# Kernel tuning notes

Hardware: AMD Instinct MI355X
Metric: run time of the kernel (lower is better)

The kernel has to match this reference:

```python
import jax, jax.numpy as jnp
import numpy as np

INPUT_SIZE = 256
HIDDEN_SIZE = 512
OUTPUT_SIZE = 256
SEQ_LEN = 32768


def setup_inputs() -> dict:
    key = jax.random.key(0)
    k_x, k_wx, k_wh, k_wy = jax.random.split(key, 4)
    x = jax.random.normal(k_x, (SEQ_LEN, INPUT_SIZE), dtype=jnp.float32)
    Wx = jax.random.normal(k_wx, (HIDDEN_SIZE, INPUT_SIZE), dtype=jnp.float32) * np.sqrt(2.0 / (INPUT_SIZE + HIDDEN_SIZE))
    Wh = jax.random.normal(k_wh, (HIDDEN_SIZE, HIDDEN_SIZE), dtype=jnp.float32) * np.sqrt(1.0 / HIDDEN_SIZE)
    Wy = jax.random.normal(k_wy, (OUTPUT_SIZE, HIDDEN_SIZE), dtype=jnp.float32) * np.sqrt(2.0 / (HIDDEN_SIZE + OUTPUT_SIZE))
    bh = jnp.zeros((HIDDEN_SIZE, 1), dtype=jnp.float32)
    by = jnp.zeros((OUTPUT_SIZE, 1), dtype=jnp.float32)
    return {"x": x, "Wx": Wx, "Wh": Wh, "Wy": Wy, "bh": bh, "by": by}


def reference(x, Wx, Wh, Wy, bh, by):
    # x: [T, I]; Wx: [H, I]; Wh: [H, H]; Wy: [O, H]; bh: [H,1]; by: [O,1]
    bh_v = bh[:, 0]  # [H]
    by_v = by[:, 0]  # [O]
    h0 = jnp.zeros((Wh.shape[0],), dtype=x.dtype)

    def step(h, x_t):
        # h_t = tanh(Wx @ x_t + Wh @ h_{t-1} + bh)
        h_new = jnp.tanh(Wx @ x_t + Wh @ h + bh_v)
        return h_new, h_new

    _, h_hist = jax.lax.scan(step, h0, x)  # [T, H]
    # y_t = Wy @ h_t + by, concatenated and flattened -> [T * O]
    y = h_hist @ Wy.T + by_v  # [T, O]
    return y.reshape(-1)
```

## Files before the change

### kernel.cpp

```cpp
#include <hip/hip_runtime.h>

#define SEQ 32768
#define ISZ 256
#define HSZ 512
#define OSZ 256
#define NLAUNCH 64
#define RTHREADS 512
#define SENT 0x7FAAAAAAu
#define KFAST 8
#define LATCH_T 48

typedef unsigned long long u64;
typedef _Float16 half2_t __attribute__((ext_vector_type(2)));

#if defined(__has_builtin)
#if __has_builtin(__builtin_amdgcn_fdot2)
#define HAVE_FDOT2 1
#endif
#endif

__device__ __forceinline__ float dot2f(half2_t a, half2_t b, float c) {
#ifdef HAVE_FDOT2
  return __builtin_amdgcn_fdot2(a, b, c, false);
#else
  return fmaf((float)a.x, (float)b.x, fmaf((float)a.y, (float)b.y, c));
#endif
}
__device__ __forceinline__ half2_t bch2(unsigned u) {
  return __builtin_bit_cast(half2_t, u);
}
__device__ __forceinline__ unsigned pkrtz_u(float x, float y) {
  return __builtin_bit_cast(unsigned, __builtin_amdgcn_cvt_pkrtz(x, y));
}

__global__ __launch_bounds__(256) void gemm_bt_bias(
    const float* __restrict__ A, const float* __restrict__ W,
    const float* __restrict__ bias, float* __restrict__ C,
    int M, int N, int K)
{
  __shared__ float As[32][68];
  __shared__ float Bs[32][68];
  const int tx = threadIdx.x;
  const int tn = tx & 15, tm = tx >> 4;
  const int m0 = blockIdx.x * 64, n0 = blockIdx.y * 64;
  const int kl = tx & 31;
  const int rl = tx >> 5;
  float acc[4][4] = {};

  for (int kt = 0; kt < K; kt += 32) {
#pragma unroll
    for (int i = 0; i < 8; ++i) {
      int m = rl + i * 8;
      As[kl][m] = A[(size_t)(m0 + m) * K + kt + kl];
      Bs[kl][m] = W[(size_t)(n0 + m) * K + kt + kl];
    }
    __syncthreads();
#pragma unroll
    for (int k = 0; k < 32; ++k) {
      float a[4], b[4];
#pragma unroll
      for (int i = 0; i < 4; ++i) a[i] = As[k][tm * 4 + i];
#pragma unroll
      for (int j = 0; j < 4; ++j) b[j] = Bs[k][tn * 4 + j];
#pragma unroll
      for (int i = 0; i < 4; ++i)
#pragma unroll
        for (int j = 0; j < 4; ++j)
          acc[i][j] = fmaf(a[i], b[j], acc[i][j]);
    }
    __syncthreads();
  }
#pragma unroll
  for (int i = 0; i < 4; ++i) {
    int m = m0 + tm * 4 + i;
#pragma unroll
    for (int j = 0; j < 4; ++j) {
      int n = n0 + tn * 4 + j;
      C[(size_t)m * N + n] = acc[i][j] + bias[n];
    }
  }
}

__device__ __forceinline__ float poll_sent(const float* p, unsigned sent) {
  float a, b;
  asm volatile(
      "s_waitcnt vmcnt(0)\n\t"
      "global_load_dword %0, %2, off sc0 sc1\n\t"
      "global_load_dword %1, %2, off sc0 sc1\n"
      "1:\n\t"
      "s_waitcnt vmcnt(1)\n\t"
      "v_cmp_eq_u32 vcc, %3, %0\n\t"
      "s_cbranch_vccz 3f\n\t"
      "global_load_dword %0, %2, off sc0 sc1\n\t"
      "s_waitcnt vmcnt(1)\n\t"
      "v_cmp_eq_u32 vcc, %3, %1\n\t"
      "s_cbranch_vccz 2f\n\t"
      "global_load_dword %1, %2, off sc0 sc1\n\t"
      "s_branch 1b\n"
      "2:\n\t"
      "v_mov_b32 %0, %1\n"
      "3:\n\t"
      "s_waitcnt vmcnt(0)"
      : "=&v"(a), "=&v"(b)
      : "v"(p), "v"(sent)
      : "memory", "vcc");
  return a;
}

__device__ __forceinline__ u64 load_fast(const u64* p) {
  u64 v;
  asm volatile("global_load_dwordx2 %0, %1, off sc0\n\t"
               "s_waitcnt vmcnt(0)"
               : "=v"(v) : "v"(p) : "memory");
  return v;
}
__device__ __forceinline__ void store_fast(u64* p, u64 v) {
  asm volatile("global_store_dwordx2 %0, %1, off sc0" :: "v"(p), "v"(v)
               : "memory");
}

__global__ __launch_bounds__(RTHREADS, 2) void rnn_recur(
    const float* __restrict__ P,
    const float* __restrict__ Wh,
    float* __restrict__ h_hist,
    u64* __restrict__ fring,
    int* __restrict__ elect)
{
  const int tid = threadIdx.x;
  const int w = tid >> 6;
  const int l = tid & 63;

  __shared__ float part[2][8][64];
  __shared__ int s_role;

  if (tid == 0) {
    unsigned xcc;
    asm volatile("s_getreg_b32 %0, hwreg(HW_REG_XCC_ID)" : "=s"(xcc));
    xcc &= 7u;
    int role = -1;
    int r = __hip_atomic_fetch_add(&elect[xcc], 1, __ATOMIC_RELAXED,
                                   __HIP_MEMORY_SCOPE_AGENT);
    if (r < 8) {
      if (r == 7) {
        int exp_ = -1;
        (void)__hip_atomic_compare_exchange_strong(
            &elect[8], &exp_, (int)xcc,
            __ATOMIC_RELEASE, __ATOMIC_RELAXED, __HIP_MEMORY_SCOPE_AGENT);
      }
      int wv;
      do {
        wv = __hip_atomic_load(&elect[8], __ATOMIC_ACQUIRE,
                               __HIP_MEMORY_SCOPE_AGENT);
      } while (wv < 0);
      if (wv == (int)xcc) role = r;
    }
    s_role = role;
  }
  __syncthreads();
  const int g = s_role;
  if (g < 0) return;

  const int g64 = g << 6;
  const int row = g64 + l;
  const int kbase = w << 6;

  unsigned wreg[32];
  {
    const float2* ws = (const float2*)(Wh + (size_t)row * HSZ + kbase);
#pragma unroll
    for (int j = 0; j < 32; ++j) {
      float2 f = ws[j];
      unsigned u = pkrtz_u(f.x, f.y);
      asm("" : "+v"(u));
      wreg[j] = u;
    }
  }

  const bool home = (w == g);
  float hreg = 0.f;
  float pv = home ? P[row] : 0.f;
  float pvn = 0.f;
  int fastok = 0, use_fast = 1;

  for (int t = 0; t < SEQ; ++t) {
    float vh = 0.f;
    if (home) {
      vh = hreg;
    } else if (t > 0) {
      int got = 0;
      if (use_fast) {
        const u64* fp = fring + (((size_t)g * 4 + (t & 3)) * 8 + w) * 64 + l;
        for (int k = 0; k < KFAST; ++k) {
          u64 v = load_fast(fp);
          if (__all((int)((unsigned)(v >> 32) == (unsigned)t))) {
            vh = __uint_as_float((unsigned)v);
            got = 1;
            break;
          }
        }
        if (t <= LATCH_T) {
          fastok += got;
          if (t == LATCH_T && fastok < LATCH_T - 8) use_fast = 0;
        }
      }
      if (!got)
        vh = poll_sent(h_hist + (size_t)t * HSZ + kbase + l, SENT);
    }

    float vn = __shfl_xor(vh, 1);
    unsigned hpu = pkrtz_u(vh, vn);
    float a0 = 0.f, a1 = 0.f, a2 = 0.f, a3 = 0.f;
#pragma unroll
    for (int j = 0; j < 8; ++j) {
      a0 = dot2f(bch2(wreg[4 * j + 0]),
                 bch2(__builtin_amdgcn_readlane(hpu, 8 * j + 0)), a0);
      a1 = dot2f(bch2(wreg[4 * j + 1]),
                 bch2(__builtin_amdgcn_readlane(hpu, 8 * j + 2)), a1);
      a2 = dot2f(bch2(wreg[4 * j + 2]),
                 bch2(__builtin_amdgcn_readlane(hpu, 8 * j + 4)), a2);
      a3 = dot2f(bch2(wreg[4 * j + 3]),
                 bch2(__builtin_amdgcn_readlane(hpu, 8 * j + 6)), a3);
    }
    part[t & 1][w][l] = (a0 + a1) + (a2 + a3);

    __syncthreads();

    if (home) {
      pvn = P[(size_t)(t + 1 < SEQ ? t + 1 : SEQ - 1) * HSZ + row];
      const int buf = t & 1;
      float p0 = part[buf][0][l], p1 = part[buf][1][l];
      float p2 = part[buf][2][l], p3 = part[buf][3][l];
      float p4 = part[buf][4][l], p5 = part[buf][5][l];
      float p6 = part[buf][6][l], p7 = part[buf][7][l];
      float s = ((p0 + p1) + (p2 + p3)) + ((p4 + p5) + (p6 + p7));
      float xv = s + pv;
      xv = fminf(fmaxf(xv, -15.f), 15.f);
      float e = __expf(2.f * xv);
      float hn = fmaf(-2.f, __builtin_amdgcn_rcpf(e + 1.f), 1.f);
      hreg = hn;
      const u64 pk = ((u64)(unsigned)(t + 1) << 32) | (u64)__float_as_uint(hn);
      const int slot = (t + 1) & 3;
#pragma unroll
      for (int j = 0; j < 8; ++j)
        store_fast(fring + (((size_t)j * 4 + slot) * 8 + g) * 64 + l, pk);
      __hip_atomic_store(&h_hist[(size_t)(t + 1) * HSZ + row], hn,
                         __ATOMIC_RELAXED, __HIP_MEMORY_SCOPE_AGENT);
      pv = pvn;
    }
  }
}

extern "C" void kernel_launch(void* const* d_in, const int* in_sizes, int n_in,
                              void* d_out, int out_size, void* d_ws, size_t ws_size,
                              hipStream_t stream) {
  const float* x  = (const float*)d_in[0];
  const float* Wx = (const float*)d_in[1];
  const float* Wh = (const float*)d_in[2];
  const float* Wy = (const float*)d_in[3];
  const float* bh = (const float*)d_in[4];
  const float* by = (const float*)d_in[5];
  float* out = (float*)d_out;

  float* P      = (float*)d_ws;
  float* h_hist = P + (size_t)SEQ * HSZ;
  u64*   fring  = (u64*)(h_hist + (size_t)(SEQ + 1) * HSZ);
  int*   elect  = (int*)(fring + (size_t)8 * 4 * 8 * 64);

  (void)hipMemsetD32Async((hipDeviceptr_t)h_hist, (int)SENT,
                          (size_t)(SEQ + 1) * HSZ, stream);
  (void)hipMemsetAsync(h_hist, 0, HSZ * sizeof(float), stream);
  (void)hipMemsetAsync(fring, 0, (size_t)8 * 4 * 8 * 64 * sizeof(u64), stream);
  (void)hipMemsetAsync(elect, 0, 8 * sizeof(int), stream);
  (void)hipMemsetAsync(elect + 8, 0xFF, sizeof(int), stream);

  gemm_bt_bias<<<dim3(SEQ / 64, HSZ / 64), dim3(256), 0, stream>>>(
      x, Wx, bh, P, SEQ, HSZ, ISZ);

  rnn_recur<<<dim3(NLAUNCH), dim3(RTHREADS), 0, stream>>>(
      P, Wh, h_hist, fring, elect);

  gemm_bt_bias<<<dim3(SEQ / 64, OSZ / 64), dim3(256), 0, stream>>>(
      h_hist + HSZ, Wy, by, out, SEQ, OSZ, HSZ);
}
```

Before: 29.30 ms.

## Exchange partial sums instead of hidden states to remove per-step block barrier

Each wave now publishes its partial dot product, tagged with the step, to a global ring. Every consumer wave gathers the eight partials for its rows, adds them and applies tanh itself. This replaces the shared-memory reduction plus __syncthreads and the separate home-wave broadcast, so one cross-block hop and one intra-block barrier drop out of the serial critical path. The sentinel-polled h_hist fallback becomes a second tagged ring read with agent-scope atomics, and the large sentinel memset goes away. In exchange, every wave now issues eight loads per step, ring traffic grows, and the tanh work is done redundantly.

```diff
diff --git a/kernel.cpp b/kernel.cpp
--- a/kernel.cpp
+++ b/kernel.cpp
@@ -6,7 +6,6 @@
 #define OSZ 256
 #define NLAUNCH 64
 #define RTHREADS 512
-#define SENT 0x7FAAAAAAu
 #define KFAST 8
 #define LATCH_T 48
 
@@ -31,6 +30,9 @@
 }
 __device__ __forceinline__ unsigned pkrtz_u(float x, float y) {
   return __builtin_bit_cast(unsigned, __builtin_amdgcn_cvt_pkrtz(x, y));
+}
+__device__ __forceinline__ float u2f(u64 v) {
+  return __uint_as_float((unsigned)v);
 }
 
 __global__ __launch_bounds__(256) void gemm_bt_bias(
@@ -81,42 +83,75 @@
   }
 }
 
-__device__ __forceinline__ float poll_sent(const float* p, unsigned sent) {
-  float a, b;
+__device__ __forceinline__ void load8_fast(const u64* p,
+    u64& a, u64& b, u64& c, u64& d, u64& e, u64& f, u64& g, u64& h) {
   asm volatile(
-      "s_waitcnt vmcnt(0)\n\t"
-      "global_load_dword %0, %2, off sc0 sc1\n\t"
-      "global_load_dword %1, %2, off sc0 sc1\n"
-      "1:\n\t"
-      "s_waitcnt vmcnt(1)\n\t"
-      "v_cmp_eq_u32 vcc, %3, %0\n\t"
-      "s_cbranch_vccz 3f\n\t"
-      "global_load_dword %0, %2, off sc0 sc1\n\t"
-      "s_waitcnt vmcnt(1)\n\t"
-      "v_cmp_eq_u32 vcc, %3, %1\n\t"
-      "s_cbranch_vccz 2f\n\t"
-      "global_load_dword %1, %2, off sc0 sc1\n\t"
-      "s_branch 1b\n"
-      "2:\n\t"
-      "v_mov_b32 %0, %1\n"
-      "3:\n\t"
+      "global_load_dwordx2 %0, %8, off sc0\n\t"
+      "global_load_dwordx2 %1, %8, off offset:512 sc0\n\t"
+      "global_load_dwordx2 %2, %8, off offset:1024 sc0\n\t"
+      "global_load_dwordx2 %3, %8, off offset:1536 sc0\n\t"
+      "global_load_dwordx2 %4, %8, off offset:2048 sc0\n\t"
+      "global_load_dwordx2 %5, %8, off offset:2560 sc0\n\t"
+      "global_load_dwordx2 %6, %8, off offset:3072 sc0\n\t"
+      "global_load_dwordx2 %7, %8, off offset:3584 sc0\n\t"
       "s_waitcnt vmcnt(0)"
-      : "=&v"(a), "=&v"(b)
-      : "v"(p), "v"(sent)
-      : "memory", "vcc");
-  return a;
-}
-
-__device__ __forceinline__ u64 load_fast(const u64* p) {
-  u64 v;
-  asm volatile("global_load_dwordx2 %0, %1, off sc0\n\t"
-               "s_waitcnt vmcnt(0)"
-               : "=v"(v) : "v"(p) : "memory");
-  return v;
+      : "=&v"(a), "=&v"(b), "=&v"(c), "=&v"(d),
+        "=&v"(e), "=&v"(f), "=&v"(g), "=&v"(h)
+      : "v"(p) : "memory");
 }
 __device__ __forceinline__ void store_fast(u64* p, u64 v) {
   asm volatile("global_store_dwordx2 %0, %1, off sc0" :: "v"(p), "v"(v)
                : "memory");
+}
+
+__device__ __forceinline__ float tanh_c(float s) {
+  float xv = fminf(fmaxf(s, -15.f), 15.f);
+  float e = __expf(2.f * xv);
+  return fmaf(-2.f, __builtin_amdgcn_rcpf(e + 1.f), 1.f);
+}
+
+__device__ __forceinline__ float acquire_sum(const u64* fb, const u64* sb,
+                                             unsigned tt, int& use_fast,
+                                             int& fastok, int tl) {
+  u64 v0 = 0, v1 = 0, v2 = 0, v3 = 0, v4 = 0, v5 = 0, v6 = 0, v7 = 0;
+  int got = 0;
+  if (use_fast) {
+    for (int k = 0; k < KFAST; ++k) {
+      load8_fast(fb, v0, v1, v2, v3, v4, v5, v6, v7);
+      int ok = ((unsigned)(v0 >> 32) == tt) & ((unsigned)(v1 >> 32) == tt) &
+               ((unsigned)(v2 >> 32) == tt) & ((unsigned)(v3 >> 32) == tt) &
+               ((unsigned)(v4 >> 32) == tt) & ((unsigned)(v5 >> 32) == tt) &
+               ((unsigned)(v6 >> 32) == tt) & ((unsigned)(v7 >> 32) == tt);
+      if (__all(ok)) { got = 1; break; }
+    }
+    if (tl <= LATCH_T) {
+      fastok += got;
+      if (tl == LATCH_T && fastok < LATCH_T - 8) use_fast = 0;
+    }
+  }
+  if (!got) {
+    for (;;) {
+      u64 x0 = __hip_atomic_load(sb + 0 * 64, __ATOMIC_RELAXED, __HIP_MEMORY_SCOPE_AGENT);
+      u64 x1 = __hip_atomic_load(sb + 1 * 64, __ATOMIC_RELAXED, __HIP_MEMORY_SCOPE_AGENT);
+      u64 x2 = __hip_atomic_load(sb + 2 * 64, __ATOMIC_RELAXED, __HIP_MEMORY_SCOPE_AGENT);
+      u64 x3 = __hip_atomic_load(sb + 3 * 64, __ATOMIC_RELAXED, __HIP_MEMORY_SCOPE_AGENT);
+      u64 x4 = __hip_atomic_load(sb + 4 * 64, __ATOMIC_RELAXED, __HIP_MEMORY_SCOPE_AGENT);
+      u64 x5 = __hip_atomic_load(sb + 5 * 64, __ATOMIC_RELAXED, __HIP_MEMORY_SCOPE_AGENT);
+      u64 x6 = __hip_atomic_load(sb + 6 * 64, __ATOMIC_RELAXED, __HIP_MEMORY_SCOPE_AGENT);
+      u64 x7 = __hip_atomic_load(sb + 7 * 64, __ATOMIC_RELAXED, __HIP_MEMORY_SCOPE_AGENT);
+      int ok = ((unsigned)(x0 >> 32) == tt) & ((unsigned)(x1 >> 32) == tt) &
+               ((unsigned)(x2 >> 32) == tt) & ((unsigned)(x3 >> 32) == tt) &
+               ((unsigned)(x4 >> 32) == tt) & ((unsigned)(x5 >> 32) == tt) &
+               ((unsigned)(x6 >> 32) == tt) & ((unsigned)(x7 >> 32) == tt);
+      if (__all(ok)) {
+        v0 = x0; v1 = x1; v2 = x2; v3 = x3;
+        v4 = x4; v5 = x5; v6 = x6; v7 = x7;
+        break;
+      }
+    }
+  }
+  return ((u2f(v0) + u2f(v1)) + (u2f(v2) + u2f(v3))) +
+         ((u2f(v4) + u2f(v5)) + (u2f(v6) + u2f(v7)));
 }
 
 __global__ __launch_bounds__(RTHREADS, 2) void rnn_recur(
@@ -124,13 +159,13 @@
     const float* __restrict__ Wh,
     float* __restrict__ h_hist,
     u64* __restrict__ fring,
+    u64* __restrict__ sring,
     int* __restrict__ elect)
 {
   const int tid = threadIdx.x;
   const int w = tid >> 6;
   const int l = tid & 63;
 
-  __shared__ float part[2][8][64];
   __shared__ int s_role;
 
   if (tid == 0) {
@@ -176,35 +211,28 @@
     }
   }
 
-  const bool home = (w == g);
-  float hreg = 0.f;
-  float pv = home ? P[row] : 0.f;
-  float pvn = 0.f;
-  int fastok = 0, use_fast = 1;
+  float pv = 0.f, pv1 = 0.f;
+  if (w == 0) {
+    pv  = P[row];
+    pv1 = P[HSZ + row];
+  }
+  int use_fast = 1, fastok = 0;
 
   for (int t = 0; t < SEQ; ++t) {
+    float pv2 = 0.f;
+    if (w == 0) {
+      int ti = t + 2 < SEQ ? t + 2 : SEQ - 1;
+      pv2 = P[(size_t)ti * HSZ + row];
+    }
+
     float vh = 0.f;
-    if (home) {
-      vh = hreg;
-    } else if (t > 0) {
-      int got = 0;
-      if (use_fast) {
-        const u64* fp = fring + (((size_t)g * 4 + (t & 3)) * 8 + w) * 64 + l;
-        for (int k = 0; k < KFAST; ++k) {
-          u64 v = load_fast(fp);
-          if (__all((int)((unsigned)(v >> 32) == (unsigned)t))) {
-            vh = __uint_as_float((unsigned)v);
-            got = 1;
-            break;
-          }
-        }
-        if (t <= LATCH_T) {
-          fastok += got;
-          if (t == LATCH_T && fastok < LATCH_T - 8) use_fast = 0;
-        }
-      }
-      if (!got)
-        vh = poll_sent(h_hist + (size_t)t * HSZ + kbase + l, SENT);
+    if (t > 0) {
+      const size_t ci = (((size_t)(t & 3) * 8 + w) * 8) * 64 + l;
+      float s8 = acquire_sum(fring + ci, sring + ci, (unsigned)t,
+                             use_fast, fastok, t);
+      vh = tanh_c(s8);
+      if (w == g)
+        h_hist[(size_t)t * HSZ + row] = vh;
     }
 
     float vn = __shfl_xor(vh, 1);
@@ -221,32 +249,25 @@
       a3 = dot2f(bch2(wreg[4 * j + 3]),
                  bch2(__builtin_amdgcn_readlane(hpu, 8 * j + 6)), a3);
     }
-    part[t & 1][w][l] = (a0 + a1) + (a2 + a3);
-
-    __syncthreads();
-
-    if (home) {
-      pvn = P[(size_t)(t + 1 < SEQ ? t + 1 : SEQ - 1) * HSZ + row];
-      const int buf = t & 1;
-      float p0 = part[buf][0][l], p1 = part[buf][1][l];
-      float p2 = part[buf][2][l], p3 = part[buf][3][l];
-      float p4 = part[buf][4][l], p5 = part[buf][5][l];
-      float p6 = part[buf][6][l], p7 = part[buf][7][l];
-      float s = ((p0 + p1) + (p2 + p3)) + ((p4 + p5) + (p6 + p7));
-      float xv = s + pv;
-      xv = fminf(fmaxf(xv, -15.f), 15.f);
-      float e = __expf(2.f * xv);
-      float hn = fmaf(-2.f, __builtin_amdgcn_rcpf(e + 1.f), 1.f);
-      hreg = hn;
-      const u64 pk = ((u64)(unsigned)(t + 1) << 32) | (u64)__float_as_uint(hn);
-      const int slot = (t + 1) & 3;
-#pragma unroll
-      for (int j = 0; j < 8; ++j)
-        store_fast(fring + (((size_t)j * 4 + slot) * 8 + g) * 64 + l, pk);
-      __hip_atomic_store(&h_hist[(size_t)(t + 1) * HSZ + row], hn,
-                         __ATOMIC_RELAXED, __HIP_MEMORY_SCOPE_AGENT);
-      pv = pvn;
-    }
+    float part = (a0 + a1) + (a2 + a3);
+    if (w == 0) {
+      part += pv;
+      pv = pv1;
+      pv1 = pv2;
+    }
+
+    const u64 pk = ((u64)(unsigned)(t + 1) << 32) | (u64)__float_as_uint(part);
+    const size_t oi = (((size_t)((t + 1) & 3) * 8 + g) * 8 + w) * 64 + l;
+    store_fast(fring + oi, pk);
+    __hip_atomic_store(sring + oi, pk, __ATOMIC_RELAXED,
+                       __HIP_MEMORY_SCOPE_AGENT);
+  }
+
+  if (w == g) {
+    const size_t ci = (((size_t)(SEQ & 3) * 8 + w) * 8) * 64 + l;
+    float s8 = acquire_sum(fring + ci, sring + ci, (unsigned)SEQ,
+                           use_fast, fastok, SEQ);
+    h_hist[(size_t)SEQ * HSZ + row] = tanh_c(s8);
   }
 }
 
@@ -264,12 +285,11 @@
   float* P      = (float*)d_ws;
   float* h_hist = P + (size_t)SEQ * HSZ;
   u64*   fring  = (u64*)(h_hist + (size_t)(SEQ + 1) * HSZ);
-  int*   elect  = (int*)(fring + (size_t)8 * 4 * 8 * 64);
-
-  (void)hipMemsetD32Async((hipDeviceptr_t)h_hist, (int)SENT,
-                          (size_t)(SEQ + 1) * HSZ, stream);
-  (void)hipMemsetAsync(h_hist, 0, HSZ * sizeof(float), stream);
-  (void)hipMemsetAsync(fring, 0, (size_t)8 * 4 * 8 * 64 * sizeof(u64), stream);
+  u64*   sring  = fring + (size_t)4 * 8 * 8 * 64;
+  int*   elect  = (int*)(sring + (size_t)4 * 8 * 8 * 64);
+
+  (void)hipMemsetAsync(fring, 0, (size_t)4 * 8 * 8 * 64 * sizeof(u64), stream);
+  (void)hipMemsetAsync(sring, 0, (size_t)4 * 8 * 8 * 64 * sizeof(u64), stream);
   (void)hipMemsetAsync(elect, 0, 8 * sizeof(int), stream);
   (void)hipMemsetAsync(elect + 8, 0xFF, sizeof(int), stream);
 
@@ -277,7 +297,7 @@
       x, Wx, bh, P, SEQ, HSZ, ISZ);
 
   rnn_recur<<<dim3(NLAUNCH), dim3(RTHREADS), 0, stream>>>(
-      P, Wh, h_hist, fring, elect);
+      P, Wh, h_hist, fring, sring, elect);
 
   gemm_bt_bias<<<dim3(SEQ / 64, OSZ / 64), dim3(256), 0, stream>>>(
       h_hist + HSZ, Wy, by, out, SEQ, OSZ, HSZ);
```

After: 48.60 ms. +65.9%, slower.
